# Optimization experiments

Hardware: AMD Instinct MI355X
Metric: run time of the kernel (lower is better)

Reference implementation:

```python
import jax, jax.numpy as jnp
import numpy as np

SCALE = 8.0  # sqrt(d_k), d_k = 64

def setup_inputs() -> dict:
    key = jax.random.key(0)
    kq, kk, kv = jax.random.split(key, 3)
    B, S, D = 32, 2048, 64
    q = jax.random.normal(kq, (B, S, D), dtype=jnp.float32)
    k = jax.random.normal(kk, (B, S, D), dtype=jnp.float32)
    v = jax.random.normal(kv, (B, S, D), dtype=jnp.float32)
    return {"q": q, "k": k, "v": v}

def reference(q, k, v):
    # scores: [B, Sq, Skv]
    scores = jnp.einsum('bqd,bkd->bqk', q, k) / SCALE
    attn = jax.nn.softmax(scores, axis=2)
    # out: [B, Sq, D]
    return jnp.einsum('bqk,bkd->bqd', attn, v)
```

## Files before the change

kernel.cpp:

```cpp
#include <hip/hip_runtime.h>

#define S_N 2048
#define D_H 64
#define KVB 64
#define NT (S_N / KVB)
#define QBLK 128
#define NBLK (32 * (S_N / QBLK))

typedef _Float16 half8 __attribute__((ext_vector_type(8)));
typedef float floatx4 __attribute__((ext_vector_type(4)));
typedef float floatx16 __attribute__((ext_vector_type(16)));
typedef unsigned int uint2v __attribute__((ext_vector_type(2)));

__device__ __forceinline__ unsigned pkh(float a, float b) {
  return __builtin_bit_cast(unsigned, __builtin_amdgcn_cvt_pkrtz(a, b));
}
__device__ __forceinline__ float bcf(unsigned u) { return __builtin_bit_cast(float, u); }
__device__ __forceinline__ unsigned bcu(float f) { return __builtin_bit_cast(unsigned, f); }

__device__ __forceinline__ int sig(int r) { return ((r & 7) + ((r >> 3) & 7)) & 7; }

__global__ __launch_bounds__(256, 2) void sdpa_kernel(
    const float* __restrict__ Q, const float* __restrict__ K,
    const float* __restrict__ V, float* __restrict__ O) {
  const int tid = threadIdx.x;
  const int wv = tid >> 6;
  const int l = tid & 63;
  const int c31 = l & 31;
  const int hi = l >> 5;

  __shared__ _Float16 KS[4][KVB * D_H];
  __shared__ _Float16 VS[4][D_H * KVB];

  const int bid = blockIdx.x;
  const int nid = (bid & 7) * (NBLK / 8) + (bid >> 3);
  const int b = nid >> 4;
  const int qt = nid & 15;

  const size_t bbase = (size_t)b * S_N * D_H;
  const int qrow = qt * QBLK + wv * 32 + c31;

  const float SCL = 0.125f * 1.44269504088896f;

  half8 qf[4];
#pragma unroll
  for (int kc = 0; kc < 4; ++kc) {
    const float* qp = Q + bbase + (size_t)qrow * D_H + kc * 16 + hi * 8;
    floatx4 x = *(const floatx4*)qp;
    floatx4 y = *(const floatx4*)(qp + 4);
    union { unsigned u[4]; half8 h; } uu = {{
        pkh(x[0] * SCL, x[1] * SCL), pkh(x[2] * SCL, x[3] * SCL),
        pkh(y[0] * SCL, y[1] * SCL), pkh(y[2] * SCL, y[3] * SCL)}};
    qf[kc] = uu.h;
  }

  const int kr_ = tid >> 3;
  const int kg8 = tid & 7;

  floatx4 kreg[2][2], vreg[2][2];

  auto loadKV = [&](int kv0) {
#pragma unroll
    for (int it = 0; it < 2; ++it) {
      const float* kp = K + bbase + (size_t)(kv0 + it * 32 + kr_) * D_H + kg8 * 8;
      kreg[it][0] = *(const floatx4*)kp;
      kreg[it][1] = *(const floatx4*)(kp + 4);
    }
#pragma unroll
    for (int r = 0; r < 2; ++r) {
      const float* vp = V + bbase + (size_t)(kv0 + 2 * kr_ + r) * D_H + kg8 * 8;
      vreg[r][0] = *(const floatx4*)vp;
      vreg[r][1] = *(const floatx4*)(vp + 4);
    }
  };

  auto writeKV = [&](int buf) {
#pragma unroll
    for (int it = 0; it < 2; ++it) {
      int row = it * 32 + kr_;
      int g = kg8 ^ sig(row);
      union { unsigned u[4]; half8 h; } uu = {{
          pkh(kreg[it][0][0], kreg[it][0][1]), pkh(kreg[it][0][2], kreg[it][0][3]),
          pkh(kreg[it][1][0], kreg[it][1][1]), pkh(kreg[it][1][2], kreg[it][1][3])}};
      *(half8*)(&KS[buf][row * 64 + g * 8]) = uu.h;
    }
#pragma unroll
    for (int jj = 0; jj < 8; ++jj) {
      int d = kg8 * 8 + jj;
      int g = (kr_ >> 2) ^ ((jj + kg8) & 7);
      unsigned val = pkh(vreg[0][jj >> 2][jj & 3], vreg[1][jj >> 2][jj & 3]);
      *(unsigned*)((char*)&VS[buf][0] + d * 128 + g * 16 + (kr_ & 3) * 4) = val;
    }
  };

  floatx16 oo[2] = {{0,0,0,0,0,0,0,0,0,0,0,0,0,0,0,0},
                    {0,0,0,0,0,0,0,0,0,0,0,0,0,0,0,0}};
  float m_ = -__builtin_inff();
  float l_ = 0.0f;

  loadKV(0);
  writeKV(0);
  __syncthreads();

  for (int t = 0; t < NT; ++t) {
    const int cur = t & 3;
    const bool pf = (t + 1) < NT;
    if (pf) loadKV((t + 1) * KVB);

    floatx16 st0 = {0,0,0,0,0,0,0,0,0,0,0,0,0,0,0,0};
    floatx16 st1 = {0,0,0,0,0,0,0,0,0,0,0,0,0,0,0,0};
    {
      const int sg0 = sig(c31), sg1 = sig(32 + c31);
      __builtin_amdgcn_s_setprio(1);
#pragma unroll
      for (int kc = 0; kc < 4; ++kc) {
        half8 kf0 = *(const half8*)(&KS[cur][c31 * 64 + (((2 * kc + hi) ^ sg0) * 8)]);
        st0 = __builtin_amdgcn_mfma_f32_32x32x16_f16(kf0, qf[kc], st0, 0, 0, 0);
        half8 kf1 = *(const half8*)(&KS[cur][(32 + c31) * 64 + (((2 * kc + hi) ^ sg1) * 8)]);
        st1 = __builtin_amdgcn_mfma_f32_32x32x16_f16(kf1, qf[kc], st1, 0, 0, 0);
      }
      __builtin_amdgcn_s_setprio(0);
    }

    float mx[8];
#pragma unroll
    for (int j = 0; j < 8; ++j)
      mx[j] = fmaxf(fmaxf(st0[j], st0[j + 8]), fmaxf(st1[j], st1[j + 8]));
    float m01 = fmaxf(mx[0], mx[1]), m23 = fmaxf(mx[2], mx[3]);
    float m45 = fmaxf(mx[4], mx[5]), m67 = fmaxf(mx[6], mx[7]);
    float tm = fmaxf(fmaxf(m01, m23), fmaxf(m45, m67));
    {
      uint2v rr = __builtin_amdgcn_permlane32_swap(bcu(tm), bcu(tm), false, false);
      tm = fmaxf(bcf(rr[0]), bcf(rr[1]));
    }
    bool skip = __all(tm <= m_ + 8.0f);
    float mn = skip ? m_ : fmaxf(m_, tm);
    float alpha = skip ? 1.0f : __builtin_amdgcn_exp2f(m_ - mn);
    m_ = mn;
#pragma unroll
    for (int r = 0; r < 16; ++r) st0[r] = __builtin_amdgcn_exp2f(st0[r] - mn);
#pragma unroll
    for (int r = 0; r < 16; ++r) st1[r] = __builtin_amdgcn_exp2f(st1[r] - mn);
    float sp[8];
#pragma unroll
    for (int j = 0; j < 8; ++j)
      sp[j] = (st0[j] + st0[j + 8]) + (st1[j] + st1[j + 8]);
    float s01 = sp[0] + sp[1], s23 = sp[2] + sp[3];
    float s45 = sp[4] + sp[5], s67 = sp[6] + sp[7];
    float ps = (s01 + s23) + (s45 + s67);
    {
      uint2v rr = __builtin_amdgcn_permlane32_swap(bcu(ps), bcu(ps), false, false);
      ps = bcf(rr[0]) + bcf(rr[1]);
    }
    if (!skip) {
      l_ *= alpha;
#pragma unroll
      for (int r = 0; r < 16; ++r) { oo[0][r] *= alpha; oo[1][r] *= alpha; }
    }
    l_ += ps;

    unsigned wds[16];
#pragma unroll
    for (int j = 0; j < 8; ++j) wds[j] = pkh(st0[2 * j], st0[2 * j + 1]);
#pragma unroll
    for (int j = 0; j < 8; ++j) wds[8 + j] = pkh(st1[2 * j], st1[2 * j + 1]);
    half8 pfrag[4];
#pragma unroll
    for (int kcc = 0; kcc < 4; ++kcc) {
      int base = (kcc >> 1) * 8 + 4 * (kcc & 1);
      uint2v r0 = __builtin_amdgcn_permlane32_swap(wds[base + 0], wds[base + 2], false, false);
      uint2v r1 = __builtin_amdgcn_permlane32_swap(wds[base + 1], wds[base + 3], false, false);
      union { unsigned u[4]; half8 h; } uu = {{r0[0], r1[0], r0[1], r1[1]}};
      pfrag[kcc] = uu.h;
    }

    if (pf) writeKV((t + 1) & 3);
    __syncthreads();

    __builtin_amdgcn_s_setprio(1);
#pragma unroll
    for (int dsub = 0; dsub < 2; ++dsub) {
      const int row = dsub * 32 + c31;
      const int sg = sig(row);
#pragma unroll
      for (int kcc = 0; kcc < 4; ++kcc) {
        half8 vf = *(const half8*)(&VS[cur][row * 64 + (((2 * kcc + hi) ^ sg) * 8)]);
        oo[dsub] = __builtin_amdgcn_mfma_f32_32x32x16_f16(vf, pfrag[kcc], oo[dsub], 0, 0, 0);
      }
    }
    __builtin_amdgcn_s_setprio(0);
  }

  float inv = 1.0f / l_;
  float* op = O + bbase + (size_t)qrow * D_H;
#pragma unroll
  for (int dsub = 0; dsub < 2; ++dsub) {
#pragma unroll
    for (int u = 0; u < 4; ++u) {
      floatx4 w;
#pragma unroll
      for (int i = 0; i < 4; ++i) w[i] = oo[dsub][4 * u + i] * inv;
      *(floatx4*)(op + dsub * 32 + u * 8 + hi * 4) = w;
    }
  }
}

extern "C" void kernel_launch(void* const* d_in, const int* in_sizes, int n_in,
                              void* d_out, int out_size, void* d_ws, size_t ws_size,
                              hipStream_t stream) {
  const float* q = (const float*)d_in[0];
  const float* k = (const float*)d_in[1];
  const float* v = (const float*)d_in[2];
  float* o = (float*)d_out;
  sdpa_kernel<<<dim3(NBLK), dim3(256), 0, stream>>>(q, k, v, o);
}
```

Measured before the change: 137.3 us.

## Double query tile to 256 rows with 512-thread blocks sharing K/V tiles

New measurement: 136.3 us. About the same (-0.7%).

```diff
diff --git a/kernel.cpp b/kernel.cpp
--- a/kernel.cpp
+++ b/kernel.cpp
@@ -4,7 +4,7 @@
 #define D_H 64
 #define KVB 64
 #define NT (S_N / KVB)
-#define QBLK 128
+#define QBLK 256
 #define NBLK (32 * (S_N / QBLK))
 
 typedef _Float16 half8 __attribute__((ext_vector_type(8)));
@@ -20,7 +20,7 @@
 
 __device__ __forceinline__ int sig(int r) { return ((r & 7) + ((r >> 3) & 7)) & 7; }
 
-__global__ __launch_bounds__(256, 2) void sdpa_kernel(
+__global__ __launch_bounds__(512, 2) void sdpa_kernel(
     const float* __restrict__ Q, const float* __restrict__ K,
     const float* __restrict__ V, float* __restrict__ O) {
   const int tid = threadIdx.x;
@@ -34,8 +34,8 @@
 
   const int bid = blockIdx.x;
   const int nid = (bid & 7) * (NBLK / 8) + (bid >> 3);
-  const int b = nid >> 4;
-  const int qt = nid & 15;
+  const int b = nid >> 3;
+  const int qt = nid & 7;
 
   const size_t bbase = (size_t)b * S_N * D_H;
   const int qrow = qt * QBLK + wv * 32 + c31;
@@ -54,42 +54,37 @@
     qf[kc] = uu.h;
   }
 
-  const int kr_ = tid >> 3;
-  const int kg8 = tid & 7;
-
-  floatx4 kreg[2][2], vreg[2][2];
+  const int r8 = tid >> 3;
+  const int g8 = tid & 7;
+  const int kvp = tid >> 4;
+  const int dc4 = tid & 15;
+
+  floatx4 kreg[2];
+  floatx4 vreg[2];
 
   auto loadKV = [&](int kv0) {
-#pragma unroll
-    for (int it = 0; it < 2; ++it) {
-      const float* kp = K + bbase + (size_t)(kv0 + it * 32 + kr_) * D_H + kg8 * 8;
-      kreg[it][0] = *(const floatx4*)kp;
-      kreg[it][1] = *(const floatx4*)(kp + 4);
-    }
-#pragma unroll
-    for (int r = 0; r < 2; ++r) {
-      const float* vp = V + bbase + (size_t)(kv0 + 2 * kr_ + r) * D_H + kg8 * 8;
-      vreg[r][0] = *(const floatx4*)vp;
-      vreg[r][1] = *(const floatx4*)(vp + 4);
-    }
+    const float* kp = K + bbase + (size_t)(kv0 + r8) * D_H + g8 * 8;
+    kreg[0] = *(const floatx4*)kp;
+    kreg[1] = *(const floatx4*)(kp + 4);
+#pragma unroll
+    for (int r = 0; r < 2; ++r)
+      vreg[r] = *(const floatx4*)(V + bbase + (size_t)(kv0 + 2 * kvp + r) * D_H + dc4 * 4);
   };
 
   auto writeKV = [&](int buf) {
-#pragma unroll
-    for (int it = 0; it < 2; ++it) {
-      int row = it * 32 + kr_;
-      int g = kg8 ^ sig(row);
+    {
+      int g = g8 ^ sig(r8);
       union { unsigned u[4]; half8 h; } uu = {{
-          pkh(kreg[it][0][0], kreg[it][0][1]), pkh(kreg[it][0][2], kreg[it][0][3]),
-          pkh(kreg[it][1][0], kreg[it][1][1]), pkh(kreg[it][1][2], kreg[it][1][3])}};
-      *(half8*)(&KS[buf][row * 64 + g * 8]) = uu.h;
-    }
-#pragma unroll
-    for (int jj = 0; jj < 8; ++jj) {
-      int d = kg8 * 8 + jj;
-      int g = (kr_ >> 2) ^ ((jj + kg8) & 7);
-      unsigned val = pkh(vreg[0][jj >> 2][jj & 3], vreg[1][jj >> 2][jj & 3]);
-      *(unsigned*)((char*)&VS[buf][0] + d * 128 + g * 16 + (kr_ & 3) * 4) = val;
+          pkh(kreg[0][0], kreg[0][1]), pkh(kreg[0][2], kreg[0][3]),
+          pkh(kreg[1][0], kreg[1][1]), pkh(kreg[1][2], kreg[1][3])}};
+      *(half8*)(&KS[buf][r8 * 64 + g * 8]) = uu.h;
+    }
+#pragma unroll
+    for (int jj = 0; jj < 4; ++jj) {
+      int d = dc4 * 4 + jj;
+      int g = (kvp >> 2) ^ (((d & 7) + ((d >> 3) & 7)) & 7);
+      unsigned val = pkh(vreg[0][jj], vreg[1][jj]);
+      *(unsigned*)((char*)&VS[buf][0] + d * 128 + g * 16 + (kvp & 3) * 4) = val;
     }
   };
 
@@ -212,5 +207,5 @@
   const float* k = (const float*)d_in[1];
   const float* v = (const float*)d_in[2];
   float* o = (float*)d_out;
-  sdpa_kernel<<<dim3(NBLK), dim3(256), 0, stream>>>(q, k, v, o);
+  sdpa_kernel<<<dim3(NBLK), dim3(512), 0, stream>>>(q, k, v, o);
 }
```
